# Kernel tuning notes

Hardware: AMD Instinct MI355X
Metric: run time of the kernel (lower is better)

The kernel has to match this reference:

```python
import jax, jax.numpy as jnp
import numpy as np

L, B, D_MODEL, N_STATE = 512, 32, 256, 16
DT_RANK = 16          # ceil(d_model / 16)
D_INNER = D_MODEL     # EXPAND = 1 (required for code self-consistency)


def setup_inputs() -> dict:
    key = jax.random.key(0)
    ks = jax.random.split(key, 6)
    return {
        "position_features": jax.random.normal(ks[0], (L, B, D_MODEL), jnp.float32),
        "flow_features": jax.random.normal(ks[1], (L, B, D_MODEL), jnp.float32),
        "h_state": jnp.zeros((B, D_INNER, N_STATE), jnp.float32),
        "x_proj_w": jax.random.normal(ks[2], (DT_RANK + 2 * N_STATE, D_INNER), jnp.float32) / np.sqrt(D_INNER).astype(np.float32),
        "dt_proj_w": jax.random.normal(ks[3], (D_INNER, DT_RANK), jnp.float32) / np.sqrt(DT_RANK).astype(np.float32),
        "dt_proj_b": jax.random.normal(ks[4], (D_INNER,), jnp.float32) * 0.01,
        "A_log": jnp.log(jnp.broadcast_to(jnp.arange(1, N_STATE + 1, dtype=jnp.float32), (D_INNER, N_STATE))),
        "D_param": jnp.ones((D_INNER,), jnp.float32),
        "out_proj_w": jax.random.normal(ks[5], (D_MODEL, D_INNER), jnp.float32) / np.sqrt(D_INNER).astype(np.float32),
    }


def _forward(position_features, flow_features, h_state,
             x_proj_w, dt_proj_w, dt_proj_b, A_log, D_param, out_proj_w):
    # permute (L, B, d) -> (B, L, d), matching forward()'s permute(1,0,2)
    u = jnp.transpose(position_features, (1, 0, 2))      # (b, l, d_in)
    flow = jnp.transpose(flow_features, (1, 0, 2))       # (b, l, d_in)

    # input-dependent delta, B, C from flow features
    x_dbl = flow @ x_proj_w.T                            # (b, l, dt_rank + 2n)
    delta, Bm, Cm = jnp.split(x_dbl, [DT_RANK, DT_RANK + N_STATE], axis=-1)
    delta = jax.nn.softplus(delta @ dt_proj_w.T + dt_proj_b)   # (b, l, d_in)

    A = -jnp.exp(A_log)                                  # (d_in, n)
    deltaA = jnp.exp(jnp.einsum('bld,dn->bldn', delta, A))         # (b,l,d,n)
    deltaB_u = jnp.einsum('bld,bln,bld->bldn', delta, Bm, u)       # (b,l,d,n)

    # sequential selective scan over l via lax.scan
    dA_t = jnp.swapaxes(deltaA, 0, 1)                    # (l, b, d, n)
    dBu_t = jnp.swapaxes(deltaB_u, 0, 1)                 # (l, b, d, n)
    C_t = jnp.swapaxes(Cm, 0, 1)                         # (l, b, n)

    def step(h, xs):
        dA, dBu, c = xs
        h = dA * h + dBu                                 # (b, d, n)
        y = jnp.einsum('bdn,bn->bd', h, c)               # (b, d)
        return h, y

    h_final, ys = jax.lax.scan(step, h_state, (dA_t, dBu_t, C_t))
    y = jnp.swapaxes(ys, 0, 1)                           # (b, l, d_in)
    y = y + u * D_param                                  # skip connection

    out = y @ out_proj_w.T                               # (b, l, d_model)
    return out.reshape(out.shape[0], -1), h_final        # flatten(1)


def reference(position_features, flow_features, h_state,
              x_proj_w, dt_proj_w, dt_proj_b, A_log, D_param, out_proj_w):
    return _forward(position_features, flow_features, h_state,
                    x_proj_w, dt_proj_w, dt_proj_b, A_log, D_param, out_proj_w)
```

## Files before the change

kernel.cpp:

```cpp
#include <hip/hip_runtime.h>
#include <hip/hip_bf16.h>

#define LL 512
#define BB 32
#define DD 256
#define NS 16
#define RK 16
#define CH 16
#define LC 32

typedef __attribute__((ext_vector_type(8))) short bf16x8;
typedef __attribute__((ext_vector_type(4))) float f32x4;

#define LD16(dst, src, off) { \
  float4 _v0 = *reinterpret_cast<const float4*>(&(src)[(off)]); \
  float4 _v1 = *reinterpret_cast<const float4*>(&(src)[(off)+4]); \
  float4 _v2 = *reinterpret_cast<const float4*>(&(src)[(off)+8]); \
  float4 _v3 = *reinterpret_cast<const float4*>(&(src)[(off)+12]); \
  dst[0]=_v0.x; dst[1]=_v0.y; dst[2]=_v0.z; dst[3]=_v0.w; \
  dst[4]=_v1.x; dst[5]=_v1.y; dst[6]=_v1.z; dst[7]=_v1.w; \
  dst[8]=_v2.x; dst[9]=_v2.y; dst[10]=_v2.z; dst[11]=_v2.w; \
  dst[12]=_v3.x; dst[13]=_v3.y; dst[14]=_v3.z; dst[15]=_v3.w; }

#define CP16(dst, src) { _Pragma("unroll") for (int _i = 0; _i < 16; ++_i) dst[_i] = src[_i]; }

static __device__ __forceinline__ unsigned short f2bf(float x) {
    __hip_bfloat16 h = __float2bfloat16(x);
    return *reinterpret_cast<unsigned short*>(&h);
}

__global__ __launch_bounds__(256) void k0_wbf(
    const float* __restrict__ W, unsigned short* __restrict__ Wbf)
{
    int i = (blockIdx.x * 256 + threadIdx.x) * 4;
    float4 v = *reinterpret_cast<const float4*>(&W[i]);
    ushort4 o;
    o.x = f2bf(v.x); o.y = f2bf(v.y); o.z = f2bf(v.z); o.w = f2bf(v.w);
    *reinterpret_cast<ushort4*>(&Wbf[i]) = o;
}

__global__ __launch_bounds__(256) void k1_proj(
    const float* __restrict__ flow,
    const float* __restrict__ x_proj_w,
    const float* __restrict__ dt_w,
    const float* __restrict__ dt_b,
    float* __restrict__ delta,
    float* __restrict__ Bm,
    float* __restrict__ Cm)
{
    const int ROWS = 32;
    const int FP = 260;
    const int SP = 49;
    __shared__ float sW[24 * FP];
    __shared__ float sflow[ROWS * FP];
    __shared__ float sdbl[ROWS * SP];
    int tid = threadIdx.x;
    int row0 = blockIdx.x * ROWS;

    #pragma unroll
    for (int jj = 0; jj < 8; ++jj) {
        int s = tid + jj * 256;
        int r = s >> 6, c4 = s & 63;
        int row = row0 + r;
        int b = row >> 9, l = row & 511;
        float4 v = *reinterpret_cast<const float4*>(&flow[(l * BB + b) * DD + c4 * 4]);
        *reinterpret_cast<float4*>(&sflow[r * FP + c4 * 4]) = v;
    }

    int r = tid >> 3, cg = tid & 7;
    const float* frow = &sflow[r * FP];

    for (int half = 0; half < 2; ++half) {
        if (half) __syncthreads();
        #pragma unroll
        for (int jj = 0; jj < 6; ++jj) {
            int s = tid + jj * 256;
            int c = s >> 6, c4 = s & 63;
            float4 v = *reinterpret_cast<const float4*>(&x_proj_w[(half * 24 + c) * DD + c4 * 4]);
            *reinterpret_cast<float4*>(&sW[c * FP + c4 * 4]) = v;
        }
        __syncthreads();

        float acc3[3] = {};
        const float* w0 = &sW[(cg * 3 + 0) * FP];
        const float* w1 = &sW[(cg * 3 + 1) * FP];
        const float* w2 = &sW[(cg * 3 + 2) * FP];
        for (int k = 0; k < DD; k += 4) {
            float4 fv = *reinterpret_cast<const float4*>(&frow[k]);
            float4 wv0 = *reinterpret_cast<const float4*>(&w0[k]);
            float4 wv1 = *reinterpret_cast<const float4*>(&w1[k]);
            float4 wv2 = *reinterpret_cast<const float4*>(&w2[k]);
            acc3[0] = fmaf(fv.x, wv0.x, acc3[0]); acc3[0] = fmaf(fv.y, wv0.y, acc3[0]);
            acc3[0] = fmaf(fv.z, wv0.z, acc3[0]); acc3[0] = fmaf(fv.w, wv0.w, acc3[0]);
            acc3[1] = fmaf(fv.x, wv1.x, acc3[1]); acc3[1] = fmaf(fv.y, wv1.y, acc3[1]);
            acc3[1] = fmaf(fv.z, wv1.z, acc3[1]); acc3[1] = fmaf(fv.w, wv1.w, acc3[1]);
            acc3[2] = fmaf(fv.x, wv2.x, acc3[2]); acc3[2] = fmaf(fv.y, wv2.y, acc3[2]);
            acc3[2] = fmaf(fv.z, wv2.z, acc3[2]); acc3[2] = fmaf(fv.w, wv2.w, acc3[2]);
        }
        #pragma unroll
        for (int j = 0; j < 3; ++j) sdbl[r * SP + half * 24 + cg * 3 + j] = acc3[j];
    }
    __syncthreads();

    #pragma unroll
    for (int jj = 0; jj < 2; ++jj) {
        int idx = tid + jj * 256;
        int rr = idx >> 4, c = idx & 15;
        Bm[(row0 + rr) * NS + c] = sdbl[rr * SP + RK + c];
        Cm[(row0 + rr) * NS + c] = sdbl[rr * SP + RK + NS + c];
    }

    float wreg[RK];
    #pragma unroll
    for (int k = 0; k < RK; k += 4) {
        float4 v = *reinterpret_cast<const float4*>(&dt_w[tid * RK + k]);
        wreg[k] = v.x; wreg[k + 1] = v.y; wreg[k + 2] = v.z; wreg[k + 3] = v.w;
    }
    float bias = dt_b[tid];
    for (int rr = 0; rr < ROWS; ++rr) {
        const float* srow = &sdbl[rr * SP];
        float s = bias;
        #pragma unroll
        for (int k = 0; k < RK; ++k) s = fmaf(srow[k], wreg[k], s);
        float sp = fmaxf(s, 0.f) + log1pf(__expf(-fabsf(s)));
        delta[(size_t)(row0 + rr) * DD + tid] = sp;
    }
}

__global__ __launch_bounds__(256) void k2_scanA(
    const float* __restrict__ u_pos,
    const float* __restrict__ A_log,
    const float* __restrict__ delta,
    const float* __restrict__ Bm,
    float* __restrict__ aprod,
    float* __restrict__ hpart)
{
    int b = blockIdx.x >> 4;
    int c = blockIdx.x & 15;
    int d = threadIdx.x;
    int l0 = c * LC;

    float a[NS];
    #pragma unroll
    for (int n = 0; n < NS; n += 4) {
        float4 v = *reinterpret_cast<const float4*>(&A_log[d * NS + n]);
        a[n]     = -__expf(v.x) * 1.44269504f;
        a[n + 1] = -__expf(v.y) * 1.44269504f;
        a[n + 2] = -__expf(v.z) * 1.44269504f;
        a[n + 3] = -__expf(v.w) * 1.44269504f;
    }
    float h[NS], ap[NS];
    #pragma unroll
    for (int n = 0; n < NS; ++n) { h[n] = 0.f; ap[n] = 1.f; }

    const float* dp = delta + ((size_t)b * LL + l0) * DD + d;
    const float* up = u_pos + ((size_t)l0 * BB + b) * DD + d;
    const float* Bp = Bm + ((size_t)b * LL + l0) * NS;

    float d0 = dp[0], d1 = dp[DD];
    float u0 = up[0], u1 = up[BB * DD];
    float B0[NS], B1[NS];
    LD16(B0, Bp, 0);
    LD16(B1, Bp, NS);

    for (int l = 0; l < LC; l += 2) {
        int lp = (l + 2 < LC) ? l + 2 : l;
        float d0n = dp[lp * DD],      d1n = dp[(lp + 1) * DD];
        float u0n = up[lp * BB * DD], u1n = up[(lp + 1) * BB * DD];
        float B0n[NS], B1n[NS];
        LD16(B0n, Bp, lp * NS);
        LD16(B1n, Bp, (lp + 1) * NS);

        float du0 = d0 * u0, du1 = d1 * u1;
        #pragma unroll
        for (int n = 0; n < NS; ++n) {
            float dA = exp2f(d0 * a[n]);
            ap[n] *= dA;
            h[n] = fmaf(dA, h[n], du0 * B0[n]);
        }
        #pragma unroll
        for (int n = 0; n < NS; ++n) {
            float dA = exp2f(d1 * a[n]);
            ap[n] *= dA;
            h[n] = fmaf(dA, h[n], du1 * B1[n]);
        }
        d0 = d0n; d1 = d1n; u0 = u0n; u1 = u1n;
        CP16(B0, B0n); CP16(B1, B1n);
    }

    size_t o = (((size_t)b * CH + c) * DD + d) * NS;
    #pragma unroll
    for (int n = 0; n < NS; n += 4) {
        *reinterpret_cast<float4*>(&aprod[o + n]) = make_float4(ap[n], ap[n+1], ap[n+2], ap[n+3]);
        *reinterpret_cast<float4*>(&hpart[o + n]) = make_float4(h[n], h[n+1], h[n+2], h[n+3]);
    }
}

__global__ __launch_bounds__(256) void k2_scanB(
    const float* __restrict__ h0,
    const float* __restrict__ aprod,
    float* __restrict__ hpart,
    float* __restrict__ h_out)
{
    int t = blockIdx.x * 256 + threadIdx.x;
    float s = h0[t];
    int b = t >> 12, dn = t & 4095;
    for (int c = 0; c < CH; ++c) {
        size_t idx = ((size_t)(b * CH + c) << 12) + dn;
        float apv = aprod[idx];
        float hpv = hpart[idx];
        hpart[idx] = s;
        s = fmaf(apv, s, hpv);
    }
    h_out[t] = s;
}

__global__ __launch_bounds__(256) void k2_scanC(
    const float* __restrict__ u_pos,
    const float* __restrict__ A_log,
    const float* __restrict__ Dp,
    const float* __restrict__ delta,
    const float* __restrict__ Bm,
    const float* __restrict__ Cm,
    const float* __restrict__ hpart,
    unsigned short* __restrict__ ybf)
{
    int b = blockIdx.x >> 4;
    int c = blockIdx.x & 15;
    int d = threadIdx.x;
    int l0 = c * LC;

    float a[NS];
    #pragma unroll
    for (int n = 0; n < NS; n += 4) {
        float4 v = *reinterpret_cast<const float4*>(&A_log[d * NS + n]);
        a[n]     = -__expf(v.x) * 1.44269504f;
        a[n + 1] = -__expf(v.y) * 1.44269504f;
        a[n + 2] = -__expf(v.z) * 1.44269504f;
        a[n + 3] = -__expf(v.w) * 1.44269504f;
    }
    float h[NS];
    {
        size_t o = (((size_t)b * CH + c) * DD + d) * NS;
        LD16(h, hpart, o);
    }
    float Dd = Dp[d];

    const float* dp = delta + ((size_t)b * LL + l0) * DD + d;
    const float* up = u_pos + ((size_t)l0 * BB + b) * DD + d;
    const float* Bp = Bm + ((size_t)b * LL + l0) * NS;
    const float* Cp = Cm + ((size_t)b * LL + l0) * NS;
    unsigned short* yp = ybf + ((size_t)b * LL + l0) * DD + d;

    float d0 = dp[0], d1 = dp[DD];
    float u0 = up[0], u1 = up[BB * DD];
    float B0[NS], B1[NS], C0[NS], C1[NS];
    LD16(B0, Bp, 0);
    LD16(B1, Bp, NS);
    LD16(C0, Cp, 0);
    LD16(C1, Cp, NS);

    for (int l = 0; l < LC; l += 2) {
        int lp = (l + 2 < LC) ? l + 2 : l;
        float d0n = dp[lp * DD],      d1n = dp[(lp + 1) * DD];
        float u0n = up[lp * BB * DD], u1n = up[(lp + 1) * BB * DD];
        float B0n[NS], B1n[NS], C0n[NS], C1n[NS];
        LD16(B0n, Bp, lp * NS);
        LD16(B1n, Bp, (lp + 1) * NS);
        LD16(C0n, Cp, lp * NS);
        LD16(C1n, Cp, (lp + 1) * NS);

        float du0 = d0 * u0, du1 = d1 * u1;
        float acc0 = 0.f, acc1 = 0.f;
        #pragma unroll
        for (int n = 0; n < NS; ++n) {
            float dA = exp2f(d0 * a[n]);
            h[n] = fmaf(dA, h[n], du0 * B0[n]);
            acc0 = fmaf(h[n], C0[n], acc0);
        }
        #pragma unroll
        for (int n = 0; n < NS; ++n) {
            float dA = exp2f(d1 * a[n]);
            h[n] = fmaf(dA, h[n], du1 * B1[n]);
            acc1 = fmaf(h[n], C1[n], acc1);
        }
        yp[l * DD]       = f2bf(fmaf(u0, Dd, acc0));
        yp[(l + 1) * DD] = f2bf(fmaf(u1, Dd, acc1));

        d0 = d0n; d1 = d1n; u0 = u0n; u1 = u1n;
        CP16(B0, B0n); CP16(B1, B1n); CP16(C0, C0n); CP16(C1, C1n);
    }
}

__global__ __launch_bounds__(256) void k3_mfma(
    const unsigned short* __restrict__ Ybf,
    const unsigned short* __restrict__ Wbf,
    float* __restrict__ Out)
{
    int wave = threadIdx.x >> 6;
    int lane = threadIdx.x & 63;
    int row0 = (blockIdx.x >> 1) * 128 + (wave >> 1) * 64;
    int col0 = (blockIdx.x & 1) * 128 + (wave & 1) * 64;
    int rl = lane & 15, kb = lane >> 4;

    f32x4 acc[4][4] = {};
    bf16x8 af[4], bf[4], afn[4], bfn[4];

    #pragma unroll
    for (int i = 0; i < 4; ++i)
        af[i] = *reinterpret_cast<const bf16x8*>(&Ybf[(size_t)(row0 + i * 16 + rl) * DD + kb * 8]);
    #pragma unroll
    for (int j = 0; j < 4; ++j)
        bf[j] = *reinterpret_cast<const bf16x8*>(&Wbf[(size_t)(col0 + j * 16 + rl) * DD + kb * 8]);

    #pragma unroll
    for (int ks = 0; ks < 8; ++ks) {
        int kn = (ks + 1) * 32 + kb * 8;
        if (ks < 7) {
            #pragma unroll
            for (int i = 0; i < 4; ++i)
                afn[i] = *reinterpret_cast<const bf16x8*>(&Ybf[(size_t)(row0 + i * 16 + rl) * DD + kn]);
            #pragma unroll
            for (int j = 0; j < 4; ++j)
                bfn[j] = *reinterpret_cast<const bf16x8*>(&Wbf[(size_t)(col0 + j * 16 + rl) * DD + kn]);
        }
        #pragma unroll
        for (int i = 0; i < 4; ++i)
            #pragma unroll
            for (int j = 0; j < 4; ++j)
                acc[i][j] = __builtin_amdgcn_mfma_f32_16x16x32_bf16(af[i], bf[j], acc[i][j], 0, 0, 0);
        #pragma unroll
        for (int i = 0; i < 4; ++i) { af[i] = afn[i]; bf[i] = bfn[i]; }
    }

    #pragma unroll
    for (int i = 0; i < 4; ++i)
        #pragma unroll
        for (int j = 0; j < 4; ++j)
            #pragma unroll
            for (int reg = 0; reg < 4; ++reg)
                Out[(size_t)(row0 + i * 16 + kb * 4 + reg) * DD + col0 + j * 16 + rl] = acc[i][j][reg];
}

extern "C" void kernel_launch(void* const* d_in, const int* in_sizes, int n_in,
                              void* d_out, int out_size, void* d_ws, size_t ws_size,
                              hipStream_t stream) {
    const float* pos  = (const float*)d_in[0];
    const float* flow = (const float*)d_in[1];
    const float* h0   = (const float*)d_in[2];
    const float* xw   = (const float*)d_in[3];
    const float* dtw  = (const float*)d_in[4];
    const float* dtb  = (const float*)d_in[5];
    const float* alog = (const float*)d_in[6];
    const float* dpar = (const float*)d_in[7];
    const float* ow   = (const float*)d_in[8];

    float* out = (float*)d_out;

    float* ws    = (float*)d_ws;
    float* delta = ws;
    float* Bmw   = ws + 4194304;
    float* Cmw   = ws + 4456448;
    float* aprod = ws + 4718592;
    float* hpart = ws + 6815744;
    unsigned short* ybf = (unsigned short*)aprod;
    unsigned short* wbf = (unsigned short*)(ws + 8912896);

    float* h_out = out + 32 * 512 * 256;

    k0_wbf  <<<64,   256, 0, stream>>>(ow, wbf);
    k1_proj <<<512,  256, 0, stream>>>(flow, xw, dtw, dtb, delta, Bmw, Cmw);
    k2_scanA<<<512,  256, 0, stream>>>(pos, alog, delta, Bmw, aprod, hpart);
    k2_scanB<<<512,  256, 0, stream>>>(h0, aprod, hpart, h_out);
    k2_scanC<<<512,  256, 0, stream>>>(pos, alog, dpar, delta, Bmw, Cmw, hpart, ybf);
    k3_mfma <<<256,  256, 0, stream>>>(ybf, wbf, out);
}
```

Before: 191.1 us.

## Fuse three-phase chunked scan into one kernel with shared-memory carry propagation

Merges the three scan kernels into one block that handles 8 channels across 32 chunks of 16 timesteps. Chunk products and partial states are exchanged through shared memory rather than global scratch, and the inter-chunk carry runs inside the block. This removes two launches and the global round trip of aprod/hpart. The output GEMM tile is halved in rows so twice as many blocks launch. In exchange, the serial carry phase uses only 128 threads and leaves the rest idle, delta/u loads are now strided per thread and less coalesced, and register prefetching was dropped.

New measurement: 189.4 us. Within noise of the previous version (-0.9%).

```diff
diff --git a/kernel.cpp b/kernel.cpp
--- a/kernel.cpp
+++ b/kernel.cpp
@@ -6,8 +6,9 @@
 #define DD 256
 #define NS 16
 #define RK 16
-#define CH 16
-#define LC 32
+#define CH2 32
+#define LC2 16
+#define DT 8
 
 typedef __attribute__((ext_vector_type(8))) short bf16x8;
 typedef __attribute__((ext_vector_type(4))) float f32x4;
@@ -21,8 +22,6 @@
   dst[4]=_v1.x; dst[5]=_v1.y; dst[6]=_v1.z; dst[7]=_v1.w; \
   dst[8]=_v2.x; dst[9]=_v2.y; dst[10]=_v2.z; dst[11]=_v2.w; \
   dst[12]=_v3.x; dst[13]=_v3.y; dst[14]=_v3.z; dst[15]=_v3.w; }
-
-#define CP16(dst, src) { _Pragma("unroll") for (int _i = 0; _i < 16; ++_i) dst[_i] = src[_i]; }
 
 static __device__ __forceinline__ unsigned short f2bf(float x) {
     __hip_bfloat16 h = __float2bfloat16(x);
@@ -127,18 +126,26 @@
     }
 }
 
-__global__ __launch_bounds__(256) void k2_scanA(
+__global__ __launch_bounds__(256) void k2_fused(
     const float* __restrict__ u_pos,
+    const float* __restrict__ h0,
     const float* __restrict__ A_log,
+    const float* __restrict__ Dp,
     const float* __restrict__ delta,
     const float* __restrict__ Bm,
-    float* __restrict__ aprod,
-    float* __restrict__ hpart)
+    const float* __restrict__ Cm,
+    unsigned short* __restrict__ ybf,
+    float* __restrict__ h_out)
 {
-    int b = blockIdx.x >> 4;
-    int c = blockIdx.x & 15;
-    int d = threadIdx.x;
-    int l0 = c * LC;
+    __shared__ float lap[NS * CH2 * DT];
+    __shared__ float lhp[NS * CH2 * DT];
+
+    int tid = threadIdx.x;
+    int b  = blockIdx.x >> 5;
+    int dt = blockIdx.x & 31;
+    int dl = tid & 7, c = tid >> 3;
+    int d  = dt * DT + dl;
+    int l0 = c * LC2;
 
     float a[NS];
     #pragma unroll
@@ -149,28 +156,22 @@
         a[n + 2] = -__expf(v.z) * 1.44269504f;
         a[n + 3] = -__expf(v.w) * 1.44269504f;
     }
-    float h[NS], ap[NS];
-    #pragma unroll
-    for (int n = 0; n < NS; ++n) { h[n] = 0.f; ap[n] = 1.f; }
 
     const float* dp = delta + ((size_t)b * LL + l0) * DD + d;
     const float* up = u_pos + ((size_t)l0 * BB + b) * DD + d;
     const float* Bp = Bm + ((size_t)b * LL + l0) * NS;
-
-    float d0 = dp[0], d1 = dp[DD];
-    float u0 = up[0], u1 = up[BB * DD];
-    float B0[NS], B1[NS];
-    LD16(B0, Bp, 0);
-    LD16(B1, Bp, NS);
-
-    for (int l = 0; l < LC; l += 2) {
-        int lp = (l + 2 < LC) ? l + 2 : l;
-        float d0n = dp[lp * DD],      d1n = dp[(lp + 1) * DD];
-        float u0n = up[lp * BB * DD], u1n = up[(lp + 1) * BB * DD];
-        float B0n[NS], B1n[NS];
-        LD16(B0n, Bp, lp * NS);
-        LD16(B1n, Bp, (lp + 1) * NS);
-
+    const float* Cp = Cm + ((size_t)b * LL + l0) * NS;
+
+    float h[NS], ap[NS];
+    #pragma unroll
+    for (int n = 0; n < NS; ++n) { h[n] = 0.f; ap[n] = 1.f; }
+
+    for (int l = 0; l < LC2; l += 2) {
+        float d0 = dp[l * DD],        d1 = dp[(l + 1) * DD];
+        float u0 = up[l * BB * DD],   u1 = up[(l + 1) * BB * DD];
+        float B0[NS], B1[NS];
+        LD16(B0, Bp, l * NS);
+        LD16(B1, Bp, (l + 1) * NS);
         float du0 = d0 * u0, du1 = d1 * u1;
         #pragma unroll
         for (int n = 0; n < NS; ++n) {
@@ -184,91 +185,43 @@
             ap[n] *= dA;
             h[n] = fmaf(dA, h[n], du1 * B1[n]);
         }
-        d0 = d0n; d1 = d1n; u0 = u0n; u1 = u1n;
-        CP16(B0, B0n); CP16(B1, B1n);
-    }
-
-    size_t o = (((size_t)b * CH + c) * DD + d) * NS;
-    #pragma unroll
-    for (int n = 0; n < NS; n += 4) {
-        *reinterpret_cast<float4*>(&aprod[o + n]) = make_float4(ap[n], ap[n+1], ap[n+2], ap[n+3]);
-        *reinterpret_cast<float4*>(&hpart[o + n]) = make_float4(h[n], h[n+1], h[n+2], h[n+3]);
-    }
-}
-
-__global__ __launch_bounds__(256) void k2_scanB(
-    const float* __restrict__ h0,
-    const float* __restrict__ aprod,
-    float* __restrict__ hpart,
-    float* __restrict__ h_out)
-{
-    int t = blockIdx.x * 256 + threadIdx.x;
-    float s = h0[t];
-    int b = t >> 12, dn = t & 4095;
-    for (int c = 0; c < CH; ++c) {
-        size_t idx = ((size_t)(b * CH + c) << 12) + dn;
-        float apv = aprod[idx];
-        float hpv = hpart[idx];
-        hpart[idx] = s;
-        s = fmaf(apv, s, hpv);
-    }
-    h_out[t] = s;
-}
-
-__global__ __launch_bounds__(256) void k2_scanC(
-    const float* __restrict__ u_pos,
-    const float* __restrict__ A_log,
-    const float* __restrict__ Dp,
-    const float* __restrict__ delta,
-    const float* __restrict__ Bm,
-    const float* __restrict__ Cm,
-    const float* __restrict__ hpart,
-    unsigned short* __restrict__ ybf)
-{
-    int b = blockIdx.x >> 4;
-    int c = blockIdx.x & 15;
-    int d = threadIdx.x;
-    int l0 = c * LC;
-
-    float a[NS];
-    #pragma unroll
-    for (int n = 0; n < NS; n += 4) {
-        float4 v = *reinterpret_cast<const float4*>(&A_log[d * NS + n]);
-        a[n]     = -__expf(v.x) * 1.44269504f;
-        a[n + 1] = -__expf(v.y) * 1.44269504f;
-        a[n + 2] = -__expf(v.z) * 1.44269504f;
-        a[n + 3] = -__expf(v.w) * 1.44269504f;
-    }
-    float h[NS];
-    {
-        size_t o = (((size_t)b * CH + c) * DD + d) * NS;
-        LD16(h, hpart, o);
-    }
+    }
+    #pragma unroll
+    for (int n = 0; n < NS; ++n) {
+        lap[n * (CH2 * DT) + c * DT + dl] = ap[n];
+        lhp[n * (CH2 * DT) + c * DT + dl] = h[n];
+    }
+    __syncthreads();
+
+    if (tid < DT * NS) {
+        int dl2 = tid & 7, n2 = tid >> 3;
+        float s = h0[((size_t)b * DD + dt * DT + dl2) * NS + n2];
+        #pragma unroll 4
+        for (int c2 = 0; c2 < CH2; ++c2) {
+            int idx = n2 * (CH2 * DT) + c2 * DT + dl2;
+            float apv = lap[idx];
+            float hpv = lhp[idx];
+            lap[idx] = s;
+            s = fmaf(apv, s, hpv);
+        }
+        h_out[((size_t)b * DD + dt * DT + dl2) * NS + n2] = s;
+    }
+    __syncthreads();
+
+    #pragma unroll
+    for (int n = 0; n < NS; ++n)
+        h[n] = lap[n * (CH2 * DT) + c * DT + dl];
     float Dd = Dp[d];
-
-    const float* dp = delta + ((size_t)b * LL + l0) * DD + d;
-    const float* up = u_pos + ((size_t)l0 * BB + b) * DD + d;
-    const float* Bp = Bm + ((size_t)b * LL + l0) * NS;
-    const float* Cp = Cm + ((size_t)b * LL + l0) * NS;
     unsigned short* yp = ybf + ((size_t)b * LL + l0) * DD + d;
 
-    float d0 = dp[0], d1 = dp[DD];
-    float u0 = up[0], u1 = up[BB * DD];
-    float B0[NS], B1[NS], C0[NS], C1[NS];
-    LD16(B0, Bp, 0);
-    LD16(B1, Bp, NS);
-    LD16(C0, Cp, 0);
-    LD16(C1, Cp, NS);
-
-    for (int l = 0; l < LC; l += 2) {
-        int lp = (l + 2 < LC) ? l + 2 : l;
-        float d0n = dp[lp * DD],      d1n = dp[(lp + 1) * DD];
-        float u0n = up[lp * BB * DD], u1n = up[(lp + 1) * BB * DD];
-        float B0n[NS], B1n[NS], C0n[NS], C1n[NS];
-        LD16(B0n, Bp, lp * NS);
-        LD16(B1n, Bp, (lp + 1) * NS);
-        LD16(C0n, Cp, lp * NS);
-        LD16(C1n, Cp, (lp + 1) * NS);
+    for (int l = 0; l < LC2; l += 2) {
+        float d0 = dp[l * DD],        d1 = dp[(l + 1) * DD];
+        float u0 = up[l * BB * DD],   u1 = up[(l + 1) * BB * DD];
+        float B0[NS], B1[NS], C0[NS], C1[NS];
+        LD16(B0, Bp, l * NS);
+        LD16(B1, Bp, (l + 1) * NS);
+        LD16(C0, Cp, l * NS);
+        LD16(C1, Cp, (l + 1) * NS);
 
         float du0 = d0 * u0, du1 = d1 * u1;
         float acc0 = 0.f, acc1 = 0.f;
@@ -286,9 +239,6 @@
         }
         yp[l * DD]       = f2bf(fmaf(u0, Dd, acc0));
         yp[(l + 1) * DD] = f2bf(fmaf(u1, Dd, acc1));
-
-        d0 = d0n; d1 = d1n; u0 = u0n; u1 = u1n;
-        CP16(B0, B0n); CP16(B1, B1n); CP16(C0, C0n); CP16(C1, C1n);
     }
 }
 
@@ -299,15 +249,15 @@
 {
     int wave = threadIdx.x >> 6;
     int lane = threadIdx.x & 63;
-    int row0 = (blockIdx.x >> 1) * 128 + (wave >> 1) * 64;
+    int row0 = (blockIdx.x >> 1) * 64 + (wave >> 1) * 32;
     int col0 = (blockIdx.x & 1) * 128 + (wave & 1) * 64;
     int rl = lane & 15, kb = lane >> 4;
 
-    f32x4 acc[4][4] = {};
-    bf16x8 af[4], bf[4], afn[4], bfn[4];
-
-    #pragma unroll
-    for (int i = 0; i < 4; ++i)
+    f32x4 acc[2][4] = {};
+    bf16x8 af[2], bf[4], afn[2], bfn[4];
+
+    #pragma unroll
+    for (int i = 0; i < 2; ++i)
         af[i] = *reinterpret_cast<const bf16x8*>(&Ybf[(size_t)(row0 + i * 16 + rl) * DD + kb * 8]);
     #pragma unroll
     for (int j = 0; j < 4; ++j)
@@ -318,23 +268,25 @@
         int kn = (ks + 1) * 32 + kb * 8;
         if (ks < 7) {
             #pragma unroll
-            for (int i = 0; i < 4; ++i)
+            for (int i = 0; i < 2; ++i)
                 afn[i] = *reinterpret_cast<const bf16x8*>(&Ybf[(size_t)(row0 + i * 16 + rl) * DD + kn]);
             #pragma unroll
             for (int j = 0; j < 4; ++j)
                 bfn[j] = *reinterpret_cast<const bf16x8*>(&Wbf[(size_t)(col0 + j * 16 + rl) * DD + kn]);
         }
         #pragma unroll
-        for (int i = 0; i < 4; ++i)
+        for (int i = 0; i < 2; ++i)
             #pragma unroll
             for (int j = 0; j < 4; ++j)
                 acc[i][j] = __builtin_amdgcn_mfma_f32_16x16x32_bf16(af[i], bf[j], acc[i][j], 0, 0, 0);
         #pragma unroll
-        for (int i = 0; i < 4; ++i) { af[i] = afn[i]; bf[i] = bfn[i]; }
-    }
-
-    #pragma unroll
-    for (int i = 0; i < 4; ++i)
+        for (int i = 0; i < 2; ++i) af[i] = afn[i];
+        #pragma unroll
+        for (int j = 0; j < 4; ++j) bf[j] = bfn[j];
+    }
+
+    #pragma unroll
+    for (int i = 0; i < 2; ++i)
         #pragma unroll
         for (int j = 0; j < 4; ++j)
             #pragma unroll
@@ -361,17 +313,13 @@
     float* delta = ws;
     float* Bmw   = ws + 4194304;
     float* Cmw   = ws + 4456448;
-    float* aprod = ws + 4718592;
-    float* hpart = ws + 6815744;
-    unsigned short* ybf = (unsigned short*)aprod;
-    unsigned short* wbf = (unsigned short*)(ws + 8912896);
+    unsigned short* ybf = (unsigned short*)(ws + 4718592);
+    unsigned short* wbf = (unsigned short*)(ws + 6815744);
 
     float* h_out = out + 32 * 512 * 256;
 
     k0_wbf  <<<64,   256, 0, stream>>>(ow, wbf);
     k1_proj <<<512,  256, 0, stream>>>(flow, xw, dtw, dtb, delta, Bmw, Cmw);
-    k2_scanA<<<512,  256, 0, stream>>>(pos, alog, delta, Bmw, aprod, hpart);
-    k2_scanB<<<512,  256, 0, stream>>>(h0, aprod, hpart, h_out);
-    k2_scanC<<<512,  256, 0, stream>>>(pos, alog, dpar, delta, Bmw, Cmw, hpart, ybf);
-    k3_mfma <<<256,  256, 0, stream>>>(ybf, wbf, out);
-}
+    k2_fused<<<1024, 256, 0, stream>>>(pos, h0, alog, dpar, delta, Bmw, Cmw, ybf, h_out);
+    k3_mfma <<<512,  256, 0, stream>>>(ybf, wbf, out);
+}
```
